# Kernel optimization log

Hardware: AMD Instinct MI355X
Metric: run time of the kernel (lower is better)

Reference implementation:

```python
import jax, jax.numpy as jnp
import numpy as np

B, S, D, H = 8, 1024, 1024, 16
DH = D // H
LN_EPS = 1e-5


def setup_inputs() -> dict:
    key = jax.random.key(0)
    ks = jax.random.split(key, 8)
    scale = 1.0 / np.sqrt(D)
    return {
        "x": jax.random.normal(ks[0], (B, S, D), dtype=jnp.float32),
        "lengths": jax.random.randint(ks[1], (B,), 0, 1024),
        "Wq": jax.random.normal(ks[2], (D, D), dtype=jnp.float32) * scale,
        "bq": jax.random.normal(ks[3], (D,), dtype=jnp.float32) * 0.01,
        "Wk": jax.random.normal(ks[4], (D, D), dtype=jnp.float32) * scale,
        "bk": jax.random.normal(ks[5], (D,), dtype=jnp.float32) * 0.01,
        "Wv": jax.random.normal(ks[6], (D, D), dtype=jnp.float32) * scale,
        "bv": jax.random.normal(ks[7], (D,), dtype=jnp.float32) * 0.01,
        "gamma": jnp.ones((D,), dtype=jnp.float32),
        "beta": jnp.zeros((D,), dtype=jnp.float32),
    }


def _split_heads(t):
    # [B,S,D] -> permute(0,2,1) -> [B,D,S] -> view(B*H,DH,S) -> permute(0,2,1)
    # equivalent to contiguous channel-chunk head split:
    return t.reshape(B, S, H, DH).transpose(0, 2, 1, 3).reshape(B * H, S, DH)


def reference(x, lengths, Wq, bq, Wk, bk, Wv, bv, gamma, beta):
    q = _split_heads(x @ Wq.T + bq)  # [B*H, S, DH]
    k = _split_heads(x @ Wk.T + bk)
    v = _split_heads(x @ Wv.T + bv)

    # Faithful bug reproduction: lengths has B entries but Q/K/V have B*H
    # rows, so only rows 0..B-1 of the flattened (B*H) dim get zeroed.
    pos = jnp.arange(S)
    row_mask = jnp.ones((B * H, S), dtype=bool)
    row_mask = row_mask.at[:B].set(pos[None, :] < lengths[:, None])
    m = row_mask[:, :, None].astype(q.dtype)
    q, k, v = q * m, k * m, v * m

    scores = jnp.einsum("bsd,btd->bst", q, k)  # [B*H, S, S]
    scores = jnp.where(scores == 0, jnp.asarray(1e-10, scores.dtype), scores)
    scores = scores / jnp.sqrt(jnp.asarray(D, scores.dtype))  # d_k = d_model
    attn = jax.nn.softmax(scores, axis=2)
    ctx = jnp.einsum("bst,btd->bsd", attn, v)  # [B*H, S, DH]

    # merge heads: inverse of _split_heads
    ctx = ctx.reshape(B, H, S, DH).transpose(0, 2, 1, 3).reshape(B, S, D)

    out = ctx + x  # dropout p=0.0
    mu = jnp.mean(out, axis=-1, keepdims=True)
    var = jnp.var(out, axis=-1, keepdims=True)
    out = (out - mu) * jax.lax.rsqrt(var + LN_EPS) * gamma + beta
    return out
```

## Files before the change

### kernel.cpp

```cpp
#include <hip/hip_runtime.h>

#define B_ 8
#define S_ 1024
#define D_ 1024
#define H_ 16
#define DH_ 64

typedef __attribute__((ext_vector_type(4))) float f32x4;
typedef __attribute__((ext_vector_type(8))) short short8;

__device__ __forceinline__ unsigned short f32_to_bf16_rne(float f) {
    union { float f; unsigned int u; } c; c.f = f;
    unsigned int u = c.u;
    unsigned int r = u + 0x7FFFu + ((u >> 16) & 1u);
    return (unsigned short)(r >> 16);
}

__device__ __forceinline__ void gl_lds16(const unsigned short* g, const unsigned short* l) {
    __builtin_amdgcn_global_load_lds((const __attribute__((address_space(1))) unsigned int*)g,
                                     (__attribute__((address_space(3))) unsigned int*)l, 16, 0, 0);
}

__global__ __launch_bounds__(256) void cvt_all(const float* __restrict__ x,
                                               const float* __restrict__ Wq,
                                               const float* __restrict__ Wk,
                                               const float* __restrict__ Wv,
                                               unsigned short* __restrict__ xb,
                                               unsigned short* __restrict__ wb) {
    int bid = blockIdx.x;
    const float* src; unsigned short* dst; long i;
    if (bid < 4096) {
        src = x; dst = xb; i = (long)bid * 256 + threadIdx.x;
    } else {
        int wbid = bid - 4096;
        int z = wbid >> 9;
        src = (z == 0) ? Wq : ((z == 1) ? Wk : Wv);
        dst = wb + (size_t)z * D_ * D_;
        i = (long)(wbid & 511) * 256 + threadIdx.x;
    }
    const float4* s4 = reinterpret_cast<const float4*>(src) + i * 2;
    float4 a = s4[0], b = s4[1];
    short8 o;
    o[0] = (short)f32_to_bf16_rne(a.x); o[1] = (short)f32_to_bf16_rne(a.y);
    o[2] = (short)f32_to_bf16_rne(a.z); o[3] = (short)f32_to_bf16_rne(a.w);
    o[4] = (short)f32_to_bf16_rne(b.x); o[5] = (short)f32_to_bf16_rne(b.y);
    o[6] = (short)f32_to_bf16_rne(b.z); o[7] = (short)f32_to_bf16_rne(b.w);
    reinterpret_cast<short8*>(dst)[i] = o;
}

__global__ __launch_bounds__(512, 1) void gemm_qkv(const unsigned short* __restrict__ X,
                                                   const unsigned short* __restrict__ Wall,
                                                   const float* __restrict__ bq,
                                                   const float* __restrict__ bk,
                                                   const float* __restrict__ bv,
                                                   const int* __restrict__ lengths,
                                                   unsigned short* __restrict__ QKV,
                                                   unsigned short* __restrict__ Vt) {
    extern __shared__ unsigned short smem[];
    const int STG = 24576;

    const int bid = blockIdx.x;
    const int xcd = bid & 7, loc = bid >> 3;
    const int mt = xcd * 4 + (loc & 3);
    const int nt = loc >> 2;
    const int m0 = mt * 256, n0 = nt * 128;
    const int tid = threadIdx.x;
    const int lane = tid & 63;
    const int w = tid >> 6;
    const int wm = (w >> 1) * 64, wn = (w & 1) * 64;

    int aoff[2][4], boff[2][4];
    #pragma unroll
    for (int ks = 0; ks < 2; ks++)
        #pragma unroll
        for (int i = 0; i < 4; i++) {
            int arow = wm + i * 16 + (lane & 15);
            aoff[ks][i] = arow * 64 + (((ks * 4 + (lane >> 4)) ^ (arow & 7)) * 8);
            int brow = wn + i * 16 + (lane & 15);
            boff[ks][i] = brow * 64 + (((ks * 4 + (lane >> 4)) ^ (brow & 7)) * 8);
        }

    for (int z = 0; z < 3; z++) {
        const unsigned short* Wz = Wall + (size_t)z * D_ * D_;
        const float* bias = (z == 0) ? bq : ((z == 1) ? bk : bv);

        const unsigned short* xsrc[4];
        const unsigned short* wsrc[2];
        #pragma unroll
        for (int p = 0; p < 4; p++) {
            int row = p * 64 + w * 8 + (lane >> 3);
            int slot = (lane & 7) ^ (row & 7);
            xsrc[p] = &X[(size_t)(m0 + row) * D_ + slot * 8];
        }
        #pragma unroll
        for (int p = 0; p < 2; p++) {
            int row = p * 64 + w * 8 + (lane >> 3);
            int slot = (lane & 7) ^ (row & 7);
            wsrc[p] = &Wz[(size_t)(n0 + row) * D_ + slot * 8];
        }

        auto stage = [&](int s) {
            unsigned short* ab = smem + s * STG;
            #pragma unroll
            for (int p = 0; p < 4; p++) {
                gl_lds16(xsrc[p], ab + (p * 512 + w * 64) * 8);
                xsrc[p] += 64;
            }
            unsigned short* bb = ab + 16384;
            #pragma unroll
            for (int p = 0; p < 2; p++) {
                gl_lds16(wsrc[p], bb + (p * 512 + w * 64) * 8);
                wsrc[p] += 64;
            }
        };

        f32x4 acc[4][4] = {};

        __syncthreads();
        stage(0);
        stage(1);
        int cur = 0;
        for (int t = 0; t < 16; t++) {
            if (t < 15) asm volatile("s_waitcnt vmcnt(6)" ::: "memory");
            else        asm volatile("s_waitcnt vmcnt(0)" ::: "memory");
            __builtin_amdgcn_s_barrier();
            if (t < 14) stage(cur ? cur - 1 : 2);
            const unsigned short* Ab = smem + cur * STG;
            const unsigned short* Bb = Ab + 16384;
            #pragma unroll
            for (int ks = 0; ks < 2; ks++) {
                short8 af[4], bf[4];
                #pragma unroll
                for (int i = 0; i < 4; i++) {
                    af[i] = *reinterpret_cast<const short8*>(&Ab[aoff[ks][i]]);
                    bf[i] = *reinterpret_cast<const short8*>(&Bb[boff[ks][i]]);
                }
                #pragma unroll
                for (int i = 0; i < 4; i++)
                    #pragma unroll
                    for (int j = 0; j < 4; j++)
                        acc[i][j] = __builtin_amdgcn_mfma_f32_16x16x32_bf16(af[i], bf[j], acc[i][j], 0, 0, 0);
            }
            cur = (cur == 2) ? 0 : cur + 1;
        }

        if (z == 2) {
            #pragma unroll
            for (int j = 0; j < 4; j++) {
                int ncol = n0 + wn + j * 16 + (lane & 15);
                float bval = bias[ncol];
                int len = (ncol < 512) ? lengths[ncol >> 6] : (1 << 30);
                int h = ncol >> 6, dh = ncol & 63;
                #pragma unroll
                for (int i = 0; i < 4; i++) {
                    int mbase = m0 + wm + i * 16 + ((lane >> 4) << 2);
                    int b = mbase >> 10, s = mbase & 1023;
                    unsigned short v4[4];
                    #pragma unroll
                    for (int r = 0; r < 4; r++) {
                        int m = mbase + r;
                        float v = acc[i][j][r] + bval;
                        if (m < S_ && ncol < 512 && m >= len) v = 0.f;
                        v4[r] = f32_to_bf16_rne(v);
                    }
                    *reinterpret_cast<uint2*>(&Vt[((size_t)((b * 16 + h) * 64 + dh)) * S_ + s]) =
                        *reinterpret_cast<uint2*>(v4);
                }
            }
        } else {
            unsigned short* Out = QKV + (size_t)z * (B_ * S_) * D_;
            #pragma unroll
            for (int j = 0; j < 4; j++) {
                int ncol = n0 + wn + j * 16 + (lane & 15);
                float bval = bias[ncol];
                int len = (ncol < 512) ? lengths[ncol >> 6] : (1 << 30);
                #pragma unroll
                for (int i = 0; i < 4; i++) {
                    int mbase = m0 + wm + i * 16 + ((lane >> 4) << 2);
                    #pragma unroll
                    for (int r = 0; r < 4; r++) {
                        int m = mbase + r;
                        float v = acc[i][j][r] + bval;
                        if (m < S_ && ncol < 512 && m >= len) v = 0.f;
                        Out[(size_t)m * D_ + ncol] = f32_to_bf16_rne(v);
                    }
                }
            }
        }
    }
}

__global__ __launch_bounds__(256, 4) void attn_kernel(const unsigned short* __restrict__ QKV,
                                                      const unsigned short* __restrict__ Vt,
                                                      unsigned short* __restrict__ Ctxb) {
    const int id = blockIdx.x;
    const int xcd = id & 7, seq = id >> 3;
    const int qt = seq & 7;
    const int bh = ((seq >> 3) << 3) | xcd;
    const int b = bh >> 4, h = bh & 15;
    const int tid = threadIdx.x, lane = tid & 63, w = tid >> 6;
    const int qcol = lane & 15, g = lane >> 4;

    __shared__ unsigned short Ks[2][64 * 64];
    __shared__ unsigned short Vs[2][64 * 64];

    const unsigned short* Qg = QKV + (size_t)(b * S_) * D_ + h * DH_;
    const unsigned short* Kg = Qg + (size_t)(B_ * S_) * D_;
    const unsigned short* Vg = Vt + (size_t)bh * DH_ * S_;

    const int q0w = qt * 128 + w * 16;

    short8 qfA[2], qfB[2];
    {
        const unsigned short* qa = Qg + (size_t)(q0w + qcol) * D_ + g * 8;
        qfA[0] = *reinterpret_cast<const short8*>(qa);
        qfA[1] = *reinterpret_cast<const short8*>(qa + 32);
        const unsigned short* qb = Qg + (size_t)(q0w + 64 + qcol) * D_ + g * 8;
        qfB[0] = *reinterpret_cast<const short8*>(qb);
        qfB[1] = *reinterpret_cast<const short8*>(qb + 32);
    }

    float lA = 0.f, lB = 0.f;
    f32x4 caccA[4] = {}, caccB[4] = {};

    const unsigned short* kp0; const unsigned short* kp1;
    const unsigned short* vp0; const unsigned short* vp1;
    {
        int i0 = (w * 2 + 0) * 64 + lane;
        int r0 = i0 >> 3, c0 = (i0 & 7) ^ (r0 & 7);
        kp0 = Kg + (size_t)r0 * D_ + c0 * 8;
        vp0 = Vg + (size_t)r0 * S_ + c0 * 8;
        int i1 = (w * 2 + 1) * 64 + lane;
        int r1 = i1 >> 3, c1 = (i1 & 7) ^ (r1 & 7);
        kp1 = Kg + (size_t)r1 * D_ + c1 * 8;
        vp1 = Vg + (size_t)r1 * S_ + c1 * 8;
    }
    unsigned short* kd0[2] = { &Ks[0][(w * 2 + 0) * 512], &Ks[1][(w * 2 + 0) * 512] };
    unsigned short* kd1[2] = { &Ks[0][(w * 2 + 1) * 512], &Ks[1][(w * 2 + 1) * 512] };
    unsigned short* vd0[2] = { &Vs[0][(w * 2 + 0) * 512], &Vs[1][(w * 2 + 0) * 512] };
    unsigned short* vd1[2] = { &Vs[0][(w * 2 + 1) * 512], &Vs[1][(w * 2 + 1) * 512] };

    auto stage = [&](int bf) {
        gl_lds16(kp0, kd0[bf]); gl_lds16(kp1, kd1[bf]);
        gl_lds16(vp0, vd0[bf]); gl_lds16(vp1, vd1[bf]);
        kp0 += 64 * D_; kp1 += 64 * D_;
        vp0 += 64;      vp1 += 64;
    };

    const float C2 = 0.04508422004083421f;
    const float MB = 11.54156171223618f;

    union F8 { unsigned int u[4]; short8 s; };

    stage(0);
    #pragma unroll 2
    for (int t = 0; t < 16; t++) {
        __syncthreads();
        if (t < 15) stage((t + 1) & 1);
        const unsigned short* Kb = Ks[t & 1];
        const unsigned short* Vb = Vs[t & 1];

        f32x4 sA[4] = {}, sB[4] = {};
        __builtin_amdgcn_s_setprio(1);
        #pragma unroll
        for (int ks = 0; ks < 2; ks++) {
            #pragma unroll
            for (int ni = 0; ni < 4; ni++) {
                int krow = ni * 16 + qcol;
                int slot = (ks * 4 + g) ^ (krow & 7);
                short8 kf = *reinterpret_cast<const short8*>(&Kb[krow * 64 + slot * 8]);
                sA[ni] = __builtin_amdgcn_mfma_f32_16x16x32_bf16(kf, qfA[ks], sA[ni], 0, 0, 0);
                sB[ni] = __builtin_amdgcn_mfma_f32_16x16x32_bf16(kf, qfB[ks], sB[ni], 0, 0, 0);
            }
        }
        __builtin_amdgcn_s_setprio(0);

        F8 pkA0, pkA1, pkB0, pkB1;
        {
            float p[16];
            #pragma unroll
            for (int ni = 0; ni < 4; ni++)
                #pragma unroll
                for (int r = 0; r < 4; r++)
                    p[ni * 4 + r] = __builtin_amdgcn_exp2f(__builtin_fmaf(sA[ni][r], C2, -MB));
            lA += ((p[0] + p[1]) + (p[2] + p[3])) + ((p[4] + p[5]) + (p[6] + p[7]))
                + ((p[8] + p[9]) + (p[10] + p[11])) + ((p[12] + p[13]) + (p[14] + p[15]));
            unsigned int Wa[4], Wb[4];
            #pragma unroll
            for (int ni = 0; ni < 4; ni++) {
                asm("v_cvt_pk_bf16_f32 %0, %1, %2" : "=v"(Wa[ni]) : "v"(p[ni * 4 + 0]), "v"(p[ni * 4 + 1]));
                asm("v_cvt_pk_bf16_f32 %0, %1, %2" : "=v"(Wb[ni]) : "v"(p[ni * 4 + 2]), "v"(p[ni * 4 + 3]));
            }
            unsigned int a0 = Wa[0], a1 = Wa[1], b0 = Wb[0], b1 = Wb[1];
            unsigned int c0 = Wa[2], c1 = Wa[3], d0 = Wb[2], d1 = Wb[3];
            asm("v_permlane32_swap_b32 %0, %1" : "+v"(a0), "+v"(a1));
            asm("v_permlane16_swap_b32 %0, %1" : "+v"(a0), "+v"(a1));
            asm("v_permlane32_swap_b32 %0, %1" : "+v"(b0), "+v"(b1));
            asm("v_permlane16_swap_b32 %0, %1" : "+v"(b0), "+v"(b1));
            asm("v_permlane32_swap_b32 %0, %1" : "+v"(c0), "+v"(c1));
            asm("v_permlane16_swap_b32 %0, %1" : "+v"(c0), "+v"(c1));
            asm("v_permlane32_swap_b32 %0, %1" : "+v"(d0), "+v"(d1));
            asm("v_permlane16_swap_b32 %0, %1" : "+v"(d0), "+v"(d1));
            pkA0.u[0] = a0; pkA0.u[1] = b0; pkA0.u[2] = a1; pkA0.u[3] = b1;
            pkA1.u[0] = c0; pkA1.u[1] = d0; pkA1.u[2] = c1; pkA1.u[3] = d1;
        }
        {
            float p[16];
            #pragma unroll
            for (int ni = 0; ni < 4; ni++)
                #pragma unroll
                for (int r = 0; r < 4; r++)
                    p[ni * 4 + r] = __builtin_amdgcn_exp2f(__builtin_fmaf(sB[ni][r], C2, -MB));
            lB += ((p[0] + p[1]) + (p[2] + p[3])) + ((p[4] + p[5]) + (p[6] + p[7]))
                + ((p[8] + p[9]) + (p[10] + p[11])) + ((p[12] + p[13]) + (p[14] + p[15]));
            unsigned int Wa[4], Wb[4];
            #pragma unroll
            for (int ni = 0; ni < 4; ni++) {
                asm("v_cvt_pk_bf16_f32 %0, %1, %2" : "=v"(Wa[ni]) : "v"(p[ni * 4 + 0]), "v"(p[ni * 4 + 1]));
                asm("v_cvt_pk_bf16_f32 %0, %1, %2" : "=v"(Wb[ni]) : "v"(p[ni * 4 + 2]), "v"(p[ni * 4 + 3]));
            }
            unsigned int a0 = Wa[0], a1 = Wa[1], b0 = Wb[0], b1 = Wb[1];
            unsigned int c0 = Wa[2], c1 = Wa[3], d0 = Wb[2], d1 = Wb[3];
            asm("v_permlane32_swap_b32 %0, %1" : "+v"(a0), "+v"(a1));
            asm("v_permlane16_swap_b32 %0, %1" : "+v"(a0), "+v"(a1));
            asm("v_permlane32_swap_b32 %0, %1" : "+v"(b0), "+v"(b1));
            asm("v_permlane16_swap_b32 %0, %1" : "+v"(b0), "+v"(b1));
            asm("v_permlane32_swap_b32 %0, %1" : "+v"(c0), "+v"(c1));
            asm("v_permlane16_swap_b32 %0, %1" : "+v"(c0), "+v"(c1));
            asm("v_permlane32_swap_b32 %0, %1" : "+v"(d0), "+v"(d1));
            asm("v_permlane16_swap_b32 %0, %1" : "+v"(d0), "+v"(d1));
            pkB0.u[0] = a0; pkB0.u[1] = b0; pkB0.u[2] = a1; pkB0.u[3] = b1;
            pkB1.u[0] = c0; pkB1.u[1] = d0; pkB1.u[2] = c1; pkB1.u[3] = d1;
        }

        __builtin_amdgcn_s_setprio(1);
        #pragma unroll
        for (int ks = 0; ks < 2; ks++) {
            short8 pfA = ks ? pkA1.s : pkA0.s;
            short8 pfB = ks ? pkB1.s : pkB0.s;
            #pragma unroll
            for (int ni = 0; ni < 4; ni++) {
                int vrow = ni * 16 + qcol;
                int slot = (ks * 4 + g) ^ (vrow & 7);
                short8 vf = *reinterpret_cast<const short8*>(&Vb[vrow * 64 + slot * 8]);
                caccA[ni] = __builtin_amdgcn_mfma_f32_16x16x32_bf16(pfA, vf, caccA[ni], 0, 0, 0);
                caccB[ni] = __builtin_amdgcn_mfma_f32_16x16x32_bf16(pfB, vf, caccB[ni], 0, 0, 0);
            }
        }
        __builtin_amdgcn_s_setprio(0);
    }

    lA += __shfl_xor(lA, 16, 64);
    lA += __shfl_xor(lA, 32, 64);
    lB += __shfl_xor(lB, 16, 64);
    lB += __shfl_xor(lB, 32, 64);

    #pragma unroll
    for (int r = 0; r < 4; r++) {
        float la = __shfl(lA, (g << 2) + r, 64);
        float lb = __shfl(lB, (g << 2) + r, 64);
        float invA = 1.f / la, invB = 1.f / lb;
        int qrowA = q0w + (g << 2) + r;
        int qrowB = qrowA + 64;
        #pragma unroll
        for (int ni = 0; ni < 4; ni++) {
            int dh = ni * 16 + qcol;
            Ctxb[(size_t)(b * S_ + qrowA) * D_ + h * DH_ + dh] = f32_to_bf16_rne(caccA[ni][r] * invA);
            Ctxb[(size_t)(b * S_ + qrowB) * D_ + h * DH_ + dh] = f32_to_bf16_rne(caccB[ni][r] * invB);
        }
    }
}

__global__ __launch_bounds__(256) void ln_kernel(const unsigned short* __restrict__ Ctxb,
                                                 const unsigned short* __restrict__ Xb,
                                                 const float* __restrict__ gamma,
                                                 const float* __restrict__ beta,
                                                 float* __restrict__ out) {
    const int row = blockIdx.x;
    const int tid = threadIdx.x;
    const int lane = tid & 63, w = tid >> 6;

    ushort4 c4 = reinterpret_cast<const ushort4*>(Ctxb + (size_t)row * D_)[tid];
    ushort4 x4 = reinterpret_cast<const ushort4*>(Xb + (size_t)row * D_)[tid];
    float4 v;
    v.x = __uint_as_float((unsigned)c4.x << 16) + __uint_as_float((unsigned)x4.x << 16);
    v.y = __uint_as_float((unsigned)c4.y << 16) + __uint_as_float((unsigned)x4.y << 16);
    v.z = __uint_as_float((unsigned)c4.z << 16) + __uint_as_float((unsigned)x4.z << 16);
    v.w = __uint_as_float((unsigned)c4.w << 16) + __uint_as_float((unsigned)x4.w << 16);

    float s = v.x + v.y + v.z + v.w;
    float ss = v.x * v.x + v.y * v.y + v.z * v.z + v.w * v.w;
    for (int off = 1; off < 64; off <<= 1) {
        s += __shfl_xor(s, off, 64);
        ss += __shfl_xor(ss, off, 64);
    }
    __shared__ float sbuf[4], ssbuf[4];
    if (lane == 0) { sbuf[w] = s; ssbuf[w] = ss; }
    __syncthreads();
    s = sbuf[0] + sbuf[1] + sbuf[2] + sbuf[3];
    ss = ssbuf[0] + ssbuf[1] + ssbuf[2] + ssbuf[3];

    float mean = s * (1.f / D_);
    float var = ss * (1.f / D_) - mean * mean;
    float rstd = rsqrtf(var + 1e-5f);

    const float4 gm = reinterpret_cast<const float4*>(gamma)[tid];
    const float4 bt = reinterpret_cast<const float4*>(beta)[tid];
    float4 o;
    o.x = (v.x - mean) * rstd * gm.x + bt.x;
    o.y = (v.y - mean) * rstd * gm.y + bt.y;
    o.z = (v.z - mean) * rstd * gm.z + bt.z;
    o.w = (v.w - mean) * rstd * gm.w + bt.w;
    reinterpret_cast<float4*>(out + (size_t)row * D_)[tid] = o;
}

extern "C" void kernel_launch(void* const* d_in, const int* in_sizes, int n_in,
                              void* d_out, int out_size, void* d_ws, size_t ws_size,
                              hipStream_t stream) {
    const float* x       = (const float*)d_in[0];
    const int*   lengths = (const int*)d_in[1];
    const float* Wq      = (const float*)d_in[2];
    const float* bq      = (const float*)d_in[3];
    const float* Wk      = (const float*)d_in[4];
    const float* bk      = (const float*)d_in[5];
    const float* Wv      = (const float*)d_in[6];
    const float* bv      = (const float*)d_in[7];
    const float* gamma   = (const float*)d_in[8];
    const float* beta    = (const float*)d_in[9];
    float* out = (float*)d_out;

    char* ws = (char*)d_ws;
    unsigned short* xb    = (unsigned short*)(ws);
    unsigned short* Wball = (unsigned short*)(ws + 16777216);
    unsigned short* QKV   = (unsigned short*)(ws + 23068672);
    unsigned short* Vt    = (unsigned short*)(ws + 56623104);
    unsigned short* Ctxb  = (unsigned short*)(ws + 73400320);

    (void)hipFuncSetAttribute((const void*)gemm_qkv,
                              hipFuncAttributeMaxDynamicSharedMemorySize, 147456);

    cvt_all<<<5632, 256, 0, stream>>>(x, Wq, Wk, Wv, xb, Wball);

    gemm_qkv<<<256, 512, 147456, stream>>>(xb, Wball, bq, bk, bv, lengths, QKV, Vt);

    attn_kernel<<<1024, 256, 0, stream>>>(QKV, Vt, Ctxb);

    ln_kernel<<<8192, 256, 0, stream>>>(Ctxb, xb, gamma, beta, out);
}
```

Measured before the change: 130.6 us.

## Fuse Q/K/V projections into one K-loop sharing each X tile

The QKV GEMM used to loop over Q, K and V sequentially and reload the X tile for each projection. It now runs one K-loop with BK=32 that loads an X tile once and multiplies it against all three weight tiles, keeping three accumulator sets live. The LDS swizzle and stage sizes are adjusted to the narrower K-step. This cuts X traffic from global memory and LDS threefold, at the cost of tripled accumulator registers (192 floats) and the launch bound changing to 2 blocks per CU, which may cause spills or not fit in LDS.

```diff
diff --git a/kernel.cpp b/kernel.cpp
--- a/kernel.cpp
+++ b/kernel.cpp
@@ -48,7 +48,7 @@
     reinterpret_cast<short8*>(dst)[i] = o;
 }
 
-__global__ __launch_bounds__(512, 1) void gemm_qkv(const unsigned short* __restrict__ X,
+__global__ __launch_bounds__(512, 2) void gemm_qkv(const unsigned short* __restrict__ X,
                                                    const unsigned short* __restrict__ Wall,
                                                    const float* __restrict__ bq,
                                                    const float* __restrict__ bk,
@@ -57,7 +57,7 @@
                                                    unsigned short* __restrict__ QKV,
                                                    unsigned short* __restrict__ Vt) {
     extern __shared__ unsigned short smem[];
-    const int STG = 24576;
+    const int STG = 20480;
 
     const int bid = blockIdx.x;
     const int xcd = bid & 7, loc = bid >> 3;
@@ -68,123 +68,122 @@
     const int lane = tid & 63;
     const int w = tid >> 6;
     const int wm = (w >> 1) * 64, wn = (w & 1) * 64;
-
-    int aoff[2][4], boff[2][4];
+    const int g = lane >> 4;
+
+    int aoff[4];
     #pragma unroll
-    for (int ks = 0; ks < 2; ks++)
-        #pragma unroll
-        for (int i = 0; i < 4; i++) {
-            int arow = wm + i * 16 + (lane & 15);
-            aoff[ks][i] = arow * 64 + (((ks * 4 + (lane >> 4)) ^ (arow & 7)) * 8);
-            int brow = wn + i * 16 + (lane & 15);
-            boff[ks][i] = brow * 64 + (((ks * 4 + (lane >> 4)) ^ (brow & 7)) * 8);
-        }
-
-    for (int z = 0; z < 3; z++) {
-        const unsigned short* Wz = Wall + (size_t)z * D_ * D_;
-        const float* bias = (z == 0) ? bq : ((z == 1) ? bk : bv);
-
-        const unsigned short* xsrc[4];
-        const unsigned short* wsrc[2];
-        #pragma unroll
-        for (int p = 0; p < 4; p++) {
-            int row = p * 64 + w * 8 + (lane >> 3);
-            int slot = (lane & 7) ^ (row & 7);
-            xsrc[p] = &X[(size_t)(m0 + row) * D_ + slot * 8];
-        }
+    for (int i = 0; i < 4; i++) {
+        int arow = wm + i * 16 + (lane & 15);
+        aoff[i] = arow * 32 + ((g ^ ((arow >> 1) & 3)) * 8);
+    }
+    const int dB = (wn - wm) * 32;
+
+    const unsigned short* xsrc[2];
+    const unsigned short* wsrc[3];
+    #pragma unroll
+    for (int p = 0; p < 2; p++) {
+        int row = p * 128 + w * 16 + (lane >> 2);
+        int c = (lane & 3) ^ ((row >> 1) & 3);
+        xsrc[p] = &X[(size_t)(m0 + row) * D_ + c * 8];
+    }
+    {
+        int row = w * 16 + (lane >> 2);
+        int c = (lane & 3) ^ ((row >> 1) & 3);
+        const unsigned short* wb0 = &Wall[(size_t)(n0 + row) * D_ + c * 8];
+        wsrc[0] = wb0;
+        wsrc[1] = wb0 + (size_t)D_ * D_;
+        wsrc[2] = wb0 + (size_t)2 * D_ * D_;
+    }
+
+    auto stage = [&](int s) {
+        unsigned short* ab = smem + s * STG;
         #pragma unroll
         for (int p = 0; p < 2; p++) {
-            int row = p * 64 + w * 8 + (lane >> 3);
-            int slot = (lane & 7) ^ (row & 7);
-            wsrc[p] = &Wz[(size_t)(n0 + row) * D_ + slot * 8];
-        }
-
-        auto stage = [&](int s) {
-            unsigned short* ab = smem + s * STG;
-            #pragma unroll
-            for (int p = 0; p < 4; p++) {
-                gl_lds16(xsrc[p], ab + (p * 512 + w * 64) * 8);
-                xsrc[p] += 64;
-            }
-            unsigned short* bb = ab + 16384;
-            #pragma unroll
-            for (int p = 0; p < 2; p++) {
-                gl_lds16(wsrc[p], bb + (p * 512 + w * 64) * 8);
-                wsrc[p] += 64;
-            }
-        };
-
-        f32x4 acc[4][4] = {};
-
-        __syncthreads();
-        stage(0);
-        stage(1);
-        int cur = 0;
-        for (int t = 0; t < 16; t++) {
-            if (t < 15) asm volatile("s_waitcnt vmcnt(6)" ::: "memory");
-            else        asm volatile("s_waitcnt vmcnt(0)" ::: "memory");
-            __builtin_amdgcn_s_barrier();
-            if (t < 14) stage(cur ? cur - 1 : 2);
-            const unsigned short* Ab = smem + cur * STG;
-            const unsigned short* Bb = Ab + 16384;
-            #pragma unroll
-            for (int ks = 0; ks < 2; ks++) {
-                short8 af[4], bf[4];
+            gl_lds16(xsrc[p], ab + (p * 512 + w * 64) * 8);
+            xsrc[p] += 32;
+        }
+        unsigned short* bb = ab + 8192;
+        #pragma unroll
+        for (int p = 0; p < 3; p++) {
+            gl_lds16(wsrc[p], bb + (p * 512 + w * 64) * 8);
+            wsrc[p] += 32;
+        }
+    };
+
+    f32x4 acc[3][4][4] = {};
+
+    stage(0);
+    stage(1);
+    int cur = 0;
+    for (int t = 0; t < 32; t++) {
+        if (t < 31) asm volatile("s_waitcnt vmcnt(5)" ::: "memory");
+        else        asm volatile("s_waitcnt vmcnt(0)" ::: "memory");
+        __builtin_amdgcn_s_barrier();
+        if (t < 30) stage(cur ? cur - 1 : 2);
+        const unsigned short* Ab = smem + cur * STG;
+        const unsigned short* Bb = Ab + 8192 + dB;
+        short8 af[4];
+        #pragma unroll
+        for (int i = 0; i < 4; i++)
+            af[i] = *reinterpret_cast<const short8*>(&Ab[aoff[i]]);
+        #pragma unroll
+        for (int z = 0; z < 3; z++) {
+            short8 bf[4];
+            #pragma unroll
+            for (int j = 0; j < 4; j++)
+                bf[j] = *reinterpret_cast<const short8*>(&Bb[z * 4096 + aoff[j]]);
+            #pragma unroll
+            for (int i = 0; i < 4; i++)
                 #pragma unroll
-                for (int i = 0; i < 4; i++) {
-                    af[i] = *reinterpret_cast<const short8*>(&Ab[aoff[ks][i]]);
-                    bf[i] = *reinterpret_cast<const short8*>(&Bb[boff[ks][i]]);
+                for (int j = 0; j < 4; j++)
+                    acc[z][i][j] = __builtin_amdgcn_mfma_f32_16x16x32_bf16(af[i], bf[j], acc[z][i][j], 0, 0, 0);
+        }
+        cur = (cur == 2) ? 0 : cur + 1;
+    }
+
+    #pragma unroll
+    for (int z = 0; z < 2; z++) {
+        unsigned short* Out = QKV + (size_t)z * (B_ * S_) * D_;
+        const float* bias = z ? bk : bq;
+        #pragma unroll
+        for (int j = 0; j < 4; j++) {
+            int ncol = n0 + wn + j * 16 + (lane & 15);
+            float bval = bias[ncol];
+            int len = (ncol < 512) ? lengths[ncol >> 6] : (1 << 30);
+            #pragma unroll
+            for (int i = 0; i < 4; i++) {
+                int mbase = m0 + wm + i * 16 + ((lane >> 4) << 2);
+                #pragma unroll
+                for (int r = 0; r < 4; r++) {
+                    int m = mbase + r;
+                    float v = acc[z][i][j][r] + bval;
+                    if (m < S_ && ncol < 512 && m >= len) v = 0.f;
+                    Out[(size_t)m * D_ + ncol] = f32_to_bf16_rne(v);
                 }
+            }
+        }
+    }
+    {
+        #pragma unroll
+        for (int j = 0; j < 4; j++) {
+            int ncol = n0 + wn + j * 16 + (lane & 15);
+            float bval = bv[ncol];
+            int len = (ncol < 512) ? lengths[ncol >> 6] : (1 << 30);
+            int h = ncol >> 6, dh = ncol & 63;
+            #pragma unroll
+            for (int i = 0; i < 4; i++) {
+                int mbase = m0 + wm + i * 16 + ((lane >> 4) << 2);
+                int b = mbase >> 10, s = mbase & 1023;
+                unsigned short v4[4];
                 #pragma unroll
-                for (int i = 0; i < 4; i++)
-                    #pragma unroll
-                    for (int j = 0; j < 4; j++)
-                        acc[i][j] = __builtin_amdgcn_mfma_f32_16x16x32_bf16(af[i], bf[j], acc[i][j], 0, 0, 0);
-            }
-            cur = (cur == 2) ? 0 : cur + 1;
-        }
-
-        if (z == 2) {
-            #pragma unroll
-            for (int j = 0; j < 4; j++) {
-                int ncol = n0 + wn + j * 16 + (lane & 15);
-                float bval = bias[ncol];
-                int len = (ncol < 512) ? lengths[ncol >> 6] : (1 << 30);
-                int h = ncol >> 6, dh = ncol & 63;
-                #pragma unroll
-                for (int i = 0; i < 4; i++) {
-                    int mbase = m0 + wm + i * 16 + ((lane >> 4) << 2);
-                    int b = mbase >> 10, s = mbase & 1023;
-                    unsigned short v4[4];
-                    #pragma unroll
-                    for (int r = 0; r < 4; r++) {
-                        int m = mbase + r;
-                        float v = acc[i][j][r] + bval;
-                        if (m < S_ && ncol < 512 && m >= len) v = 0.f;
-                        v4[r] = f32_to_bf16_rne(v);
-                    }
-                    *reinterpret_cast<uint2*>(&Vt[((size_t)((b * 16 + h) * 64 + dh)) * S_ + s]) =
-                        *reinterpret_cast<uint2*>(v4);
+                for (int r = 0; r < 4; r++) {
+                    int m = mbase + r;
+                    float v = acc[2][i][j][r] + bval;
+                    if (m < S_ && ncol < 512 && m >= len) v = 0.f;
+                    v4[r] = f32_to_bf16_rne(v);
                 }
-            }
-        } else {
-            unsigned short* Out = QKV + (size_t)z * (B_ * S_) * D_;
-            #pragma unroll
-            for (int j = 0; j < 4; j++) {
-                int ncol = n0 + wn + j * 16 + (lane & 15);
-                float bval = bias[ncol];
-                int len = (ncol < 512) ? lengths[ncol >> 6] : (1 << 30);
-                #pragma unroll
-                for (int i = 0; i < 4; i++) {
-                    int mbase = m0 + wm + i * 16 + ((lane >> 4) << 2);
-                    #pragma unroll
-                    for (int r = 0; r < 4; r++) {
-                        int m = mbase + r;
-                        float v = acc[i][j][r] + bval;
-                        if (m < S_ && ncol < 512 && m >= len) v = 0.f;
-                        Out[(size_t)m * D_ + ncol] = f32_to_bf16_rne(v);
-                    }
-                }
+                *reinterpret_cast<uint2*>(&Vt[((size_t)((b * 16 + h) * 64 + dh)) * S_ + s]) =
+                    *reinterpret_cast<uint2*>(v4);
             }
         }
     }
@@ -437,11 +436,11 @@
     unsigned short* Ctxb  = (unsigned short*)(ws + 73400320);
 
     (void)hipFuncSetAttribute((const void*)gemm_qkv,
-                              hipFuncAttributeMaxDynamicSharedMemorySize, 147456);
+                              hipFuncAttributeMaxDynamicSharedMemorySize, 122880);
 
     cvt_all<<<5632, 256, 0, stream>>>(x, Wq, Wk, Wv, xb, Wball);
 
-    gemm_qkv<<<256, 512, 147456, stream>>>(xb, Wball, bq, bk, bv, lengths, QKV, Vt);
+    gemm_qkv<<<256, 512, 122880, stream>>>(xb, Wball, bq, bk, bv, lengths, QKV, Vt);
 
     attn_kernel<<<1024, 256, 0, stream>>>(QKV, Vt, Ctxb);
 
```

After: 137.7 us. 1.05x slower.

## Restructure QKV GEMM into 256x256 tiles with interleaved LDS staging

Applied to the files above, without the earlier changes.

The fused QKV projection switches from 256x128 tiles that loop over Q, K and V inside each block to 256x256 tiles, one projection per block, launched as 384 blocks. The K loop now uses double buffering with four MFMA phases per step. Global-to-LDS loads for the next tile are interleaved between phases, with barriers and s_setprio to overlap memory and compute. The aim is more data reuse per tile and better parallelism across the grid, at the cost of more accumulator registers and more barriers.

```diff
diff --git a/kernel.cpp b/kernel.cpp
--- a/kernel.cpp
+++ b/kernel.cpp
@@ -57,134 +57,185 @@
                                                    unsigned short* __restrict__ QKV,
                                                    unsigned short* __restrict__ Vt) {
     extern __shared__ unsigned short smem[];
-    const int STG = 24576;
 
     const int bid = blockIdx.x;
-    const int xcd = bid & 7, loc = bid >> 3;
-    const int mt = xcd * 4 + (loc & 3);
-    const int nt = loc >> 2;
-    const int m0 = mt * 256, n0 = nt * 128;
+    const int xcd = bid & 7, idx = bid >> 3;
+    const int mt = xcd * 4 + (idx & 3);
+    const int nt = idx >> 2;
+    const int m0 = mt * 256, n0 = nt * 256;
+    const int z = nt >> 2;
     const int tid = threadIdx.x;
     const int lane = tid & 63;
     const int w = tid >> 6;
-    const int wm = (w >> 1) * 64, wn = (w & 1) * 64;
-
-    int aoff[2][4], boff[2][4];
+    const int wm = (w >> 2) * 128, wn = (w & 3) * 64;
+    const int g = lane >> 4;
+
+    int aoffk[2][4], boffk[2][4];
     #pragma unroll
     for (int ks = 0; ks < 2; ks++)
         #pragma unroll
         for (int i = 0; i < 4; i++) {
-            int arow = wm + i * 16 + (lane & 15);
-            aoff[ks][i] = arow * 64 + (((ks * 4 + (lane >> 4)) ^ (arow & 7)) * 8);
-            int brow = wn + i * 16 + (lane & 15);
-            boff[ks][i] = brow * 64 + (((ks * 4 + (lane >> 4)) ^ (brow & 7)) * 8);
-        }
-
-    for (int z = 0; z < 3; z++) {
-        const unsigned short* Wz = Wall + (size_t)z * D_ * D_;
-        const float* bias = (z == 0) ? bq : ((z == 1) ? bk : bv);
-
-        const unsigned short* xsrc[4];
-        const unsigned short* wsrc[2];
-        #pragma unroll
-        for (int p = 0; p < 4; p++) {
-            int row = p * 64 + w * 8 + (lane >> 3);
-            int slot = (lane & 7) ^ (row & 7);
-            xsrc[p] = &X[(size_t)(m0 + row) * D_ + slot * 8];
-        }
-        #pragma unroll
-        for (int p = 0; p < 2; p++) {
-            int row = p * 64 + w * 8 + (lane >> 3);
-            int slot = (lane & 7) ^ (row & 7);
-            wsrc[p] = &Wz[(size_t)(n0 + row) * D_ + slot * 8];
-        }
-
-        auto stage = [&](int s) {
-            unsigned short* ab = smem + s * STG;
-            #pragma unroll
-            for (int p = 0; p < 4; p++) {
-                gl_lds16(xsrc[p], ab + (p * 512 + w * 64) * 8);
-                xsrc[p] += 64;
-            }
-            unsigned short* bb = ab + 16384;
-            #pragma unroll
-            for (int p = 0; p < 2; p++) {
-                gl_lds16(wsrc[p], bb + (p * 512 + w * 64) * 8);
-                wsrc[p] += 64;
-            }
-        };
-
-        f32x4 acc[4][4] = {};
-
-        __syncthreads();
-        stage(0);
-        stage(1);
-        int cur = 0;
-        for (int t = 0; t < 16; t++) {
-            if (t < 15) asm volatile("s_waitcnt vmcnt(6)" ::: "memory");
-            else        asm volatile("s_waitcnt vmcnt(0)" ::: "memory");
-            __builtin_amdgcn_s_barrier();
-            if (t < 14) stage(cur ? cur - 1 : 2);
-            const unsigned short* Ab = smem + cur * STG;
-            const unsigned short* Bb = Ab + 16384;
-            #pragma unroll
-            for (int ks = 0; ks < 2; ks++) {
-                short8 af[4], bf[4];
-                #pragma unroll
-                for (int i = 0; i < 4; i++) {
-                    af[i] = *reinterpret_cast<const short8*>(&Ab[aoff[ks][i]]);
-                    bf[i] = *reinterpret_cast<const short8*>(&Bb[boff[ks][i]]);
-                }
-                #pragma unroll
-                for (int i = 0; i < 4; i++)
-                    #pragma unroll
-                    for (int j = 0; j < 4; j++)
-                        acc[i][j] = __builtin_amdgcn_mfma_f32_16x16x32_bf16(af[i], bf[j], acc[i][j], 0, 0, 0);
-            }
-            cur = (cur == 2) ? 0 : cur + 1;
-        }
-
-        if (z == 2) {
-            #pragma unroll
-            for (int j = 0; j < 4; j++) {
-                int ncol = n0 + wn + j * 16 + (lane & 15);
-                float bval = bias[ncol];
-                int len = (ncol < 512) ? lengths[ncol >> 6] : (1 << 30);
-                int h = ncol >> 6, dh = ncol & 63;
-                #pragma unroll
-                for (int i = 0; i < 4; i++) {
-                    int mbase = m0 + wm + i * 16 + ((lane >> 4) << 2);
-                    int b = mbase >> 10, s = mbase & 1023;
-                    unsigned short v4[4];
-                    #pragma unroll
-                    for (int r = 0; r < 4; r++) {
-                        int m = mbase + r;
-                        float v = acc[i][j][r] + bval;
-                        if (m < S_ && ncol < 512 && m >= len) v = 0.f;
-                        v4[r] = f32_to_bf16_rne(v);
-                    }
-                    *reinterpret_cast<uint2*>(&Vt[((size_t)((b * 16 + h) * 64 + dh)) * S_ + s]) =
-                        *reinterpret_cast<uint2*>(v4);
+            int ar = wm + i * 16 + (lane & 15);
+            aoffk[ks][i] = ar * 64 + (((ks * 4 + g) ^ (lane & 7)) * 8);
+            int br = wn + i * 16 + (lane & 15);
+            boffk[ks][i] = 16384 + br * 64 + (((ks * 4 + g) ^ (lane & 7)) * 8);
+        }
+
+    const int srow = tid >> 3;
+    const int scol = (tid & 7) ^ (srow & 7);
+    const unsigned short* gA = X    + (size_t)(m0 + srow) * D_ + scol * 8;
+    const unsigned short* gB = Wall + (size_t)(n0 + srow) * D_ + scol * 8;
+
+    auto stageAq = [&](int p, int q, int kt) {
+        gl_lds16(gA + (size_t)q * 64 * D_ + kt * 64,
+                 smem + p * 32768 + q * 4096 + tid * 8);
+    };
+    auto stageBq = [&](int p, int q, int kt) {
+        gl_lds16(gB + (size_t)q * 64 * D_ + kt * 64,
+                 smem + p * 32768 + 16384 + q * 4096 + tid * 8);
+    };
+
+    #pragma unroll
+    for (int q = 0; q < 4; q++) stageAq(0, q, 0);
+    #pragma unroll
+    for (int q = 0; q < 4; q++) stageBq(0, q, 0);
+    #pragma unroll
+    for (int q = 0; q < 4; q++) stageAq(1, q, 1);
+    #pragma unroll
+    for (int q = 0; q < 4; q++) stageBq(1, q, 1);
+    asm volatile("s_waitcnt vmcnt(8)" ::: "memory");
+    __builtin_amdgcn_s_barrier();
+
+    f32x4 acc[8][4] = {};
+
+    #pragma unroll 2
+    for (int kt = 0; kt < 16; kt++) {
+        const int p = kt & 1;
+        const unsigned short* Ab = smem + p * 32768;
+        short8 af[2][4], bf[2][4];
+
+        #pragma unroll
+        for (int ks = 0; ks < 2; ks++) {
+            #pragma unroll
+            for (int i = 0; i < 4; i++)
+                af[ks][i] = *reinterpret_cast<const short8*>(&Ab[aoffk[ks][i]]);
+            #pragma unroll
+            for (int j = 0; j < 2; j++)
+                bf[ks][j] = *reinterpret_cast<const short8*>(&Ab[boffk[ks][j]]);
+        }
+        __builtin_amdgcn_s_barrier();
+        asm volatile("s_waitcnt lgkmcnt(0)" ::: "memory");
+        __builtin_amdgcn_s_setprio(1);
+        #pragma unroll
+        for (int ks = 0; ks < 2; ks++)
+            #pragma unroll
+            for (int i = 0; i < 4; i++)
+                #pragma unroll
+                for (int j = 0; j < 2; j++)
+                    acc[i][j] = __builtin_amdgcn_mfma_f32_16x16x32_bf16(af[ks][i], bf[ks][j], acc[i][j], 0, 0, 0);
+        __builtin_amdgcn_s_setprio(0);
+        __builtin_amdgcn_s_barrier();
+
+        #pragma unroll
+        for (int ks = 0; ks < 2; ks++)
+            #pragma unroll
+            for (int j = 2; j < 4; j++)
+                bf[ks][j] = *reinterpret_cast<const short8*>(&Ab[boffk[ks][j]]);
+        if (kt < 14) { stageAq(p, 0, kt + 2); stageAq(p, 2, kt + 2); }
+        __builtin_amdgcn_s_barrier();
+        asm volatile("s_waitcnt lgkmcnt(0)" ::: "memory");
+        __builtin_amdgcn_s_setprio(1);
+        #pragma unroll
+        for (int ks = 0; ks < 2; ks++)
+            #pragma unroll
+            for (int i = 0; i < 4; i++)
+                #pragma unroll
+                for (int j = 2; j < 4; j++)
+                    acc[i][j] = __builtin_amdgcn_mfma_f32_16x16x32_bf16(af[ks][i], bf[ks][j], acc[i][j], 0, 0, 0);
+        __builtin_amdgcn_s_setprio(0);
+        __builtin_amdgcn_s_barrier();
+
+        #pragma unroll
+        for (int ks = 0; ks < 2; ks++)
+            #pragma unroll
+            for (int i = 0; i < 4; i++)
+                af[ks][i] = *reinterpret_cast<const short8*>(&Ab[aoffk[ks][i] + 4096]);
+        if (kt < 14) {
+            #pragma unroll
+            for (int q = 0; q < 4; q++) stageBq(p, q, kt + 2);
+        }
+        __builtin_amdgcn_s_barrier();
+        asm volatile("s_waitcnt lgkmcnt(0)" ::: "memory");
+        __builtin_amdgcn_s_setprio(1);
+        #pragma unroll
+        for (int ks = 0; ks < 2; ks++)
+            #pragma unroll
+            for (int i = 0; i < 4; i++)
+                #pragma unroll
+                for (int j = 0; j < 2; j++)
+                    acc[4 + i][j] = __builtin_amdgcn_mfma_f32_16x16x32_bf16(af[ks][i], bf[ks][j], acc[4 + i][j], 0, 0, 0);
+        __builtin_amdgcn_s_setprio(0);
+        __builtin_amdgcn_s_barrier();
+
+        if (kt < 14) { stageAq(p, 1, kt + 2); stageAq(p, 3, kt + 2); }
+        if (kt < 15) {
+            if (kt < 14) asm volatile("s_waitcnt vmcnt(8)" ::: "memory");
+            else         asm volatile("s_waitcnt vmcnt(0)" ::: "memory");
+        }
+        __builtin_amdgcn_s_barrier();
+        __builtin_amdgcn_s_setprio(1);
+        #pragma unroll
+        for (int ks = 0; ks < 2; ks++)
+            #pragma unroll
+            for (int i = 0; i < 4; i++)
+                #pragma unroll
+                for (int j = 2; j < 4; j++)
+                    acc[4 + i][j] = __builtin_amdgcn_mfma_f32_16x16x32_bf16(af[ks][i], bf[ks][j], acc[4 + i][j], 0, 0, 0);
+        __builtin_amdgcn_s_setprio(0);
+        __builtin_amdgcn_s_barrier();
+    }
+
+    const float* bias = (z == 0) ? bq : ((z == 1) ? bk : bv);
+    if (z < 2) {
+        unsigned short* Out = QKV + (size_t)z * (B_ * S_) * D_;
+        #pragma unroll
+        for (int j = 0; j < 4; j++) {
+            int ncol = (n0 + wn + j * 16 + (lane & 15)) & 1023;
+            float bval = bias[ncol];
+            int len = (ncol < 512) ? lengths[ncol >> 6] : (1 << 30);
+            #pragma unroll
+            for (int i = 0; i < 8; i++) {
+                int mbase = m0 + wm + i * 16 + (g << 2);
+                #pragma unroll
+                for (int r = 0; r < 4; r++) {
+                    int m = mbase + r;
+                    float v = acc[i][j][r] + bval;
+                    if (m < S_ && ncol < 512 && m >= len) v = 0.f;
+                    Out[(size_t)m * D_ + ncol] = f32_to_bf16_rne(v);
                 }
             }
-        } else {
-            unsigned short* Out = QKV + (size_t)z * (B_ * S_) * D_;
-            #pragma unroll
-            for (int j = 0; j < 4; j++) {
-                int ncol = n0 + wn + j * 16 + (lane & 15);
-                float bval = bias[ncol];
-                int len = (ncol < 512) ? lengths[ncol >> 6] : (1 << 30);
-                #pragma unroll
-                for (int i = 0; i < 4; i++) {
-                    int mbase = m0 + wm + i * 16 + ((lane >> 4) << 2);
-                    #pragma unroll
-                    for (int r = 0; r < 4; r++) {
-                        int m = mbase + r;
-                        float v = acc[i][j][r] + bval;
-                        if (m < S_ && ncol < 512 && m >= len) v = 0.f;
-                        Out[(size_t)m * D_ + ncol] = f32_to_bf16_rne(v);
-                    }
+        }
+    } else {
+        #pragma unroll
+        for (int j = 0; j < 4; j++) {
+            int ncol = (n0 + wn + j * 16 + (lane & 15)) & 1023;
+            float bval = bias[ncol];
+            int len = (ncol < 512) ? lengths[ncol >> 6] : (1 << 30);
+            int h = ncol >> 6, dh = ncol & 63;
+            #pragma unroll
+            for (int i = 0; i < 8; i++) {
+                int mbase = m0 + wm + i * 16 + (g << 2);
+                int b = mbase >> 10, s = mbase & 1023;
+                unsigned short v4[4];
+                #pragma unroll
+                for (int r = 0; r < 4; r++) {
+                    int m = mbase + r;
+                    float v = acc[i][j][r] + bval;
+                    if (m < S_ && ncol < 512 && m >= len) v = 0.f;
+                    v4[r] = f32_to_bf16_rne(v);
                 }
+                *reinterpret_cast<uint2*>(&Vt[((size_t)((b * 16 + h) * 64 + dh)) * S_ + s]) =
+                    *reinterpret_cast<uint2*>(v4);
             }
         }
     }
@@ -437,11 +488,11 @@
     unsigned short* Ctxb  = (unsigned short*)(ws + 73400320);
 
     (void)hipFuncSetAttribute((const void*)gemm_qkv,
-                              hipFuncAttributeMaxDynamicSharedMemorySize, 147456);
+                              hipFuncAttributeMaxDynamicSharedMemorySize, 131072);
 
     cvt_all<<<5632, 256, 0, stream>>>(x, Wq, Wk, Wv, xb, Wball);
 
-    gemm_qkv<<<256, 512, 147456, stream>>>(xb, Wball, bq, bk, bv, lengths, QKV, Vt);
+    gemm_qkv<<<384, 512, 131072, stream>>>(xb, Wball, bq, bk, bv, lengths, QKV, Vt);
 
     attn_kernel<<<1024, 256, 0, stream>>>(QKV, Vt, Ctxb);
 
```

New measurement: 143.5 us. 1.1x slower.
